# Optimization experiments

Hardware: AMD Instinct MI355X
Metric: run time of the kernel (lower is better)

The kernel has to match this reference:

```python
import jax, jax.numpy as jnp
import numpy as np

H, W = 260, 346          # DAVIS346 sensor resolution
TEMP = 256.0             # time-decay temperature
B, T = 16, 4096          # batch, event sequence length
C = 2 * H + 2 * W        # pred channel dim = 1212


def setup_inputs() -> dict:
    key = jax.random.key(0)
    k1, k2, k3, k4, k5 = jax.random.split(key, 5)
    pred = jax.random.normal(k1, (B, T, C), dtype=jnp.float32)
    # target columns: [timestamp, y_index, x_index, polarity]
    t = jnp.sort(jax.random.uniform(k2, (B, T), minval=0.0, maxval=1.0e6), axis=1)
    y = jax.random.randint(k3, (B, T), 0, H)
    x = jax.random.randint(k4, (B, T), 0, W)
    p = jax.random.randint(k5, (B, T), 0, 2)
    target = jnp.stack([t,
                        y.astype(jnp.float32),
                        x.astype(jnp.float32),
                        p.astype(jnp.float32)], axis=-1)  # [B,T,4]
    return {"pred": pred, "target": target}


def _loss(pred, target):
    t = target[..., 0]                          # [B,T] timestamps
    y = target[..., 1].astype(jnp.int32)        # row indices
    x = target[..., 2].astype(jnp.int32)        # col indices
    p = target[..., 3]                          # polarity in {0,1}
    p_ = p[..., None]

    oh_y = jax.nn.one_hot(y, H, dtype=pred.dtype)   # [B,T,H]
    oh_x = jax.nn.one_hot(x, W, dtype=pred.dtype)   # [B,T,W]
    # scatter targets, concatenated in pred's channel layout [H0|H1|W0|W1]
    base = jnp.concatenate([oh_y * (1.0 - p_), oh_y * p_,
                            oh_x * (1.0 - p_), oh_x * p_], axis=-1)  # [B,T,C]

    # exponential time decay between consecutive events: d_i = exp(-(t_{i+1}-t_i)/TEMP)
    decay = jnp.exp(-(t[:, 1:] - t[:, :-1]) / TEMP)  # [B,T-1]

    # reverse recurrence: s_{T-1} = base_{T-1}; s_i = base_i + d_i * s_{i+1} for i = T-2..1;
    # s_0 = base_0 (torch loop stops before updating index 0)
    base_tm = jnp.swapaxes(base, 0, 1)               # [T,B,C] time-major
    decay_tm = jnp.swapaxes(decay, 0, 1)[..., None]  # [T-1,B,1]

    def step(carry, xd):
        b, d = xd
        s = b + d * carry
        return s, s

    _, ys = jax.lax.scan(step, base_tm[-1], (base_tm[:-1], decay_tm), reverse=True)
    s = jnp.concatenate([ys, base_tm[-1:]], axis=0)  # [T,B,C]
    s = s.at[0].set(base_tm[0])                      # index 0 never accumulated
    s = jnp.swapaxes(s, 0, 1)                        # [B,T,C]

    segs = [(0, H), (H, 2 * H), (2 * H, 2 * H + W), (2 * H + W, C)]
    losses = []
    for a, b in segs:
        logp = jax.nn.log_softmax(pred[..., a:b], axis=-1)
        soft = jax.nn.softmax(s[..., a:b], axis=-1)
        losses.append(-(soft * logp).sum(-1))        # soft-target CE, [B,T]
    lH0, lH1, lW0, lW1 = losses

    loss = ((lH0 + lW0) * (1.0 - p) + (lH1 + lW1) * p).mean()
    return loss


def reference(pred, target):
    return _loss(pred, target)
```

## Files before the change

### kernel.cpp

```cpp
#include <hip/hip_runtime.h>

#define HH 260
#define WW 346
#define CC 1212
#define CP 1280
#define HALF 640
#define NA 606
#define BB 16
#define TT 4096
#define INV_TEMP (1.0f/256.0f)
#define KCH 256
#define LCH 16
#define NG 16
#define GSZ 16
#define GLEN (GSZ * LCH)
#define NJ 10

__global__ __launch_bounds__(256) void p1_local(const float* __restrict__ target,
                                                float* __restrict__ Lbuf) {
    const int blk = blockIdx.x;
    const int b = blk >> 6;
    const int k0 = (blk & 63) << 2;
    const int tid = threadIdx.x;
    const int w = tid >> 6, lane = tid & 63;
    const int k = k0 + w;
    const int a = k * LCH;

    __shared__ float tg[4][LCH][4];
    __shared__ float tnextS[4];
    tg[tid >> 6][(tid >> 2) & 15][tid & 3] =
        target[((size_t)b * TT + k0 * LCH) * 4 + tid];
    if (tid < 4) {
        const int kk = k0 + tid;
        tnextS[tid] = (kk < KCH - 1) ? target[((size_t)b * TT + (kk + 1) * LCH) * 4] : 0.0f;
    }
    __syncthreads();

    float s0[NJ], s1[NJ];
#pragma unroll
    for (int j = 0; j < NJ; ++j) { s0[j] = 0.f; s1[j] = 0.f; }

    for (int li = LCH - 1; li >= 0; --li) {
        const int i = a + li;
        const float ti = tg[w][li][0];
        const float tn = (li == LCH - 1) ? tnextS[w] : tg[w][li + 1][0];
        const float d = (i >= TT - 1) ? 0.0f : __expf(-(tn - ti) * INV_TEMP);
        const int y = (int)tg[w][li][1], x = (int)tg[w][li][2], p = (int)tg[w][li][3];
        const int uy = y, ux = 260 + x;
        if (p == 0) {
#pragma unroll
            for (int j = 0; j < NJ; ++j) {
                const int u = lane + 64 * j;
                const float add = (u == uy ? 1.f : 0.f) + (u == ux ? 1.f : 0.f);
                s0[j] = fmaf(s0[j], d, add);
                s1[j] *= d;
            }
        } else {
#pragma unroll
            for (int j = 0; j < NJ; ++j) {
                const int u = lane + 64 * j;
                const float add = (u == uy ? 1.f : 0.f) + (u == ux ? 1.f : 0.f);
                s1[j] = fmaf(s1[j], d, add);
                s0[j] *= d;
            }
        }
    }
    float* __restrict__ out = Lbuf + (size_t)(b * KCH + k) * CP;
#pragma unroll
    for (int j = 0; j < NJ; ++j) {
        out[lane + 64 * j] = s0[j];
        out[HALF + lane + 64 * j] = s1[j];
    }
}

__global__ __launch_bounds__(256) void p2a(const float* __restrict__ target,
                                           const float* __restrict__ Lbuf,
                                           float* __restrict__ LCin,
                                           float* __restrict__ GroupL) {
    const int blk = blockIdx.x;
    const int ct = blk % 5;
    const int bg = blk / 5;
    const int b = bg >> 4, g = bg & 15;
    const int c = ct * 256 + threadIdx.x;

    float carry = 0.f;
#pragma unroll
    for (int kk = GSZ - 1; kk >= 0; --kk) {
        const int k = g * GSZ + kk;
        const size_t idx = ((size_t)(b * KCH + k)) * CP + c;
        LCin[idx] = carry;
        float P = 0.f;
        if (k < KCH - 1) {
            const float ta = target[((size_t)b * TT + k * LCH) * 4];
            const float te = target[((size_t)b * TT + (k + 1) * LCH) * 4];
            P = __expf(-(te - ta) * INV_TEMP);
        }
        carry = fmaf(P, carry, Lbuf[idx]);
    }
    GroupL[(size_t)bg * CP + c] = carry;
}

__global__ __launch_bounds__(256) void p2b(const float* __restrict__ target,
                                           const float* __restrict__ GroupL,
                                           float* __restrict__ SC) {
    const int blk = blockIdx.x;
    const int ct = blk % 5;
    const int b = blk / 5;
    const int c = ct * 256 + threadIdx.x;

    float Gv[NG], GP[NG];
#pragma unroll
    for (int g = 0; g < NG; ++g)
        Gv[g] = GroupL[((size_t)(b * NG + g)) * CP + c];
#pragma unroll
    for (int g = 0; g < NG; ++g) {
        if (g < NG - 1) {
            const float ta = target[((size_t)b * TT + g * GLEN) * 4];
            const float te = target[((size_t)b * TT + (g + 1) * GLEN) * 4];
            GP[g] = __expf(-(te - ta) * INV_TEMP);
        } else GP[g] = 0.f;
    }
    float carry = 0.f;
#pragma unroll
    for (int g = NG - 1; g >= 0; --g) {
        SC[((size_t)(b * NG + g)) * CP + c] = carry;
        carry = fmaf(GP[g], carry, Gv[g]);
    }
}

__global__ __launch_bounds__(256, 6) void p3_loss(const float* __restrict__ pred,
                                                  const float* __restrict__ target,
                                                  const float* __restrict__ LCin,
                                                  const float* __restrict__ SC,
                                                  double* __restrict__ partials) {
    const int blk = blockIdx.x;
    const int b = blk >> 6;
    const int k0 = (blk & 63) << 2;
    const int tid = threadIdx.x;
    const int w = tid >> 6, lane = tid & 63;
    const int k = k0 + w;
    const int g = k >> 4;
    const int a = k * LCH;

    __shared__ float tg[4][LCH][4];
    __shared__ float tnextS[4];
    tg[tid >> 6][(tid >> 2) & 15][tid & 3] =
        target[((size_t)b * TT + k0 * LCH) * 4 + tid];
    if (tid < 4) {
        const int kk = k0 + tid;
        tnextS[tid] = (kk < KCH - 1) ? target[((size_t)b * TT + (kk + 1) * LCH) * 4] : 0.0f;
    }
    __syncthreads();

    float Qk = 0.f;
    if (g < NG - 1) {
        const float tge = target[((size_t)b * TT + (g + 1) * GLEN) * 4];
        const float tk1 = target[((size_t)b * TT + (k + 1) * LCH) * 4];
        Qk = __expf(-(tge - tk1) * INV_TEMP);
    }

    const float* __restrict__ lc = LCin + (size_t)(b * KCH + k) * CP;
    const float* __restrict__ sc = SC + ((size_t)(b * NG + g)) * CP;
    float s0[NJ], s1[NJ];
#pragma unroll
    for (int j = 0; j < NJ; ++j) {
        const int u = lane + 64 * j;
        s0[j] = fmaf(Qk, sc[u], lc[u]);
        s1[j] = fmaf(Qk, sc[HALF + u], lc[HALF + u]);
    }

    float prA[NJ], prB[NJ];
    {
        const int p = (int)tg[w][LCH - 1][3];
        const float* __restrict__ prow = pred + ((size_t)b * TT + a + LCH - 1) * CC;
#pragma unroll
        for (int j = 0; j < NJ; ++j) {
            const int u = lane + 64 * j;
            const int c = (u < 260) ? p * HH + u : 2 * HH + p * WW + (u - 260);
            prA[j] = (u < NA) ? prow[c] : 0.0f;
        }
    }

    double lacc = 0.0;
    for (int li = LCH - 1; li >= 0; --li) {
        if (li > 0) {
            const int pn = (int)tg[w][li - 1][3];
            const float* __restrict__ prow = pred + ((size_t)b * TT + a + li - 1) * CC;
#pragma unroll
            for (int j = 0; j < NJ; ++j) {
                const int u = lane + 64 * j;
                const int c = (u < 260) ? pn * HH + u : 2 * HH + pn * WW + (u - 260);
                prB[j] = (u < NA) ? prow[c] : 0.0f;
            }
        }

        const int i = a + li;
        const float ti = tg[w][li][0];
        const float tn = (li == LCH - 1) ? tnextS[w] : tg[w][li + 1][0];
        const float d = (i == 0 || i >= TT - 1) ? 0.0f : __expf(-(tn - ti) * INV_TEMP);
        const int y = (int)tg[w][li][1], x = (int)tg[w][li][2], p = (int)tg[w][li][3];
        const int uy = y, ux = 260 + x;

        float zpy = 0.f, zsy = 0.f, dty = 0.f;
        float zpx = 0.f, zsx = 0.f, dtx = 0.f;

        auto stepActive = [&](float (&SA)[NJ], float (&SO)[NJ]) {
#pragma unroll
            for (int j = 0; j < NJ; ++j) {
                const int u = lane + 64 * j;
                const float add = (u == uy ? 1.f : 0.f) + (u == ux ? 1.f : 0.f);
                SA[j] = fmaf(SA[j], d, add);
                SO[j] *= d;
                float es = __expf(SA[j]);
                float ep = __expf(prA[j]);
                if (j == NJ - 1) {
                    const float m = (u < NA) ? 1.f : 0.f;
                    es *= m; ep *= m;
                }
                if (j < 4) {
                    zpy += ep; zsy += es; dty = fmaf(es, prA[j], dty);
                } else if (j == 4) {
                    const bool isY = (u < 260);
                    zpy += isY ? ep : 0.f;
                    zsy += isY ? es : 0.f;
                    dty = fmaf(isY ? es : 0.f, prA[j], dty);
                    zpx += isY ? 0.f : ep;
                    zsx += isY ? 0.f : es;
                    dtx = fmaf(isY ? 0.f : es, prA[j], dtx);
                } else {
                    zpx += ep; zsx += es; dtx = fmaf(es, prA[j], dtx);
                }
            }
        };
        if (p == 0) stepActive(s0, s1); else stepActive(s1, s0);

#pragma unroll
        for (int off = 32; off > 0; off >>= 1) {
            zpy += __shfl_xor(zpy, off);
            zsy += __shfl_xor(zsy, off);
            dty += __shfl_xor(dty, off);
            zpx += __shfl_xor(zpx, off);
            zsx += __shfl_xor(zsx, off);
            dtx += __shfl_xor(dtx, off);
        }
        const float loss = __logf(zpy) + __logf(zpx)
                         - __fdividef(dty, zsy) - __fdividef(dtx, zsx);
        lacc += (double)loss;

#pragma unroll
        for (int j = 0; j < NJ; ++j) prA[j] = prB[j];
    }
    if (lane == 0) partials[b * KCH + k] = lacc;
}

__global__ void p4_final(const double* __restrict__ partials, float* __restrict__ out) {
    const int tid = threadIdx.x;
    double sum = 0.0;
    for (int i = tid; i < BB * KCH; i += 256) sum += partials[i];
#pragma unroll
    for (int off = 32; off > 0; off >>= 1) sum += __shfl_xor(sum, off);
    __shared__ double sred[4];
    if ((tid & 63) == 0) sred[tid >> 6] = sum;
    __syncthreads();
    if (tid == 0)
        out[0] = (float)((sred[0] + sred[1] + sred[2] + sred[3]) / (double)((size_t)BB * TT));
}

extern "C" void kernel_launch(void* const* d_in, const int* in_sizes, int n_in,
                              void* d_out, int out_size, void* d_ws, size_t ws_size,
                              hipStream_t stream) {
    const float* pred   = (const float*)d_in[0];
    const float* target = (const float*)d_in[1];
    float* out = (float*)d_out;

    double* partials = (double*)d_ws;
    float* Lbuf   = (float*)((char*)d_ws + 65536);
    float* LCin   = Lbuf + (size_t)BB * KCH * CP;
    float* GroupL = LCin + (size_t)BB * KCH * CP;
    float* SC     = GroupL + (size_t)BB * NG * CP;

    p1_local<<<BB * KCH / 4, 256, 0, stream>>>(target, Lbuf);
    p2a<<<BB * NG * 5, 256, 0, stream>>>(target, Lbuf, LCin, GroupL);
    p2b<<<BB * 5, 256, 0, stream>>>(target, GroupL, SC);
    p3_loss<<<BB * KCH / 4, 256, 0, stream>>>(pred, target, LCin, SC, partials);
    p4_final<<<1, 256, 0, stream>>>(partials, out);
}
```

Before: 82.13 us.

## Split loss kernel by polarity across a second grid dimension

The loss kernel now launches twice as many blocks, one per polarity half of the state. Each block keeps only one 640-wide state half in registers and processes only the events whose polarity matches its half, decaying the state for the others. The software prefetch of the next pred row is removed and pred is loaded inline. The aim is to halve register state, raise occupancy (launch bounds go from 6 to 8) and give more parallelism, at the cost of exposed pred load latency and possible divergence from data-dependent skipping.

```diff
diff --git a/kernel.cpp b/kernel.cpp
--- a/kernel.cpp
+++ b/kernel.cpp
@@ -128,12 +128,13 @@
     }
 }
 
-__global__ __launch_bounds__(256, 6) void p3_loss(const float* __restrict__ pred,
+__global__ __launch_bounds__(256, 8) void p3_loss(const float* __restrict__ pred,
                                                   const float* __restrict__ target,
                                                   const float* __restrict__ LCin,
                                                   const float* __restrict__ SC,
                                                   double* __restrict__ partials) {
     const int blk = blockIdx.x;
+    const int q = blockIdx.y;
     const int b = blk >> 6;
     const int k0 = (blk & 63) << 2;
     const int tid = threadIdx.x;
@@ -159,80 +160,61 @@
         Qk = __expf(-(tge - tk1) * INV_TEMP);
     }
 
-    const float* __restrict__ lc = LCin + (size_t)(b * KCH + k) * CP;
-    const float* __restrict__ sc = SC + ((size_t)(b * NG + g)) * CP;
-    float s0[NJ], s1[NJ];
+    const float* __restrict__ lc = LCin + (size_t)(b * KCH + k) * CP + q * HALF;
+    const float* __restrict__ sc = SC + ((size_t)(b * NG + g)) * CP + q * HALF;
+    float s[NJ];
 #pragma unroll
     for (int j = 0; j < NJ; ++j) {
         const int u = lane + 64 * j;
-        s0[j] = fmaf(Qk, sc[u], lc[u]);
-        s1[j] = fmaf(Qk, sc[HALF + u], lc[HALF + u]);
-    }
-
-    float prA[NJ], prB[NJ];
-    {
-        const int p = (int)tg[w][LCH - 1][3];
-        const float* __restrict__ prow = pred + ((size_t)b * TT + a + LCH - 1) * CC;
-#pragma unroll
-        for (int j = 0; j < NJ; ++j) {
-            const int u = lane + 64 * j;
-            const int c = (u < 260) ? p * HH + u : 2 * HH + p * WW + (u - 260);
-            prA[j] = (u < NA) ? prow[c] : 0.0f;
-        }
+        s[j] = fmaf(Qk, sc[u], lc[u]);
     }
 
     double lacc = 0.0;
     for (int li = LCH - 1; li >= 0; --li) {
-        if (li > 0) {
-            const int pn = (int)tg[w][li - 1][3];
-            const float* __restrict__ prow = pred + ((size_t)b * TT + a + li - 1) * CC;
-#pragma unroll
-            for (int j = 0; j < NJ; ++j) {
-                const int u = lane + 64 * j;
-                const int c = (u < 260) ? pn * HH + u : 2 * HH + pn * WW + (u - 260);
-                prB[j] = (u < NA) ? prow[c] : 0.0f;
-            }
-        }
-
         const int i = a + li;
         const float ti = tg[w][li][0];
         const float tn = (li == LCH - 1) ? tnextS[w] : tg[w][li + 1][0];
         const float d = (i == 0 || i >= TT - 1) ? 0.0f : __expf(-(tn - ti) * INV_TEMP);
         const int y = (int)tg[w][li][1], x = (int)tg[w][li][2], p = (int)tg[w][li][3];
+
+        if (p != q) {
+#pragma unroll
+            for (int j = 0; j < NJ; ++j) s[j] *= d;
+            continue;
+        }
+
         const int uy = y, ux = 260 + x;
+        const float* __restrict__ prow = pred + ((size_t)b * TT + i) * CC;
 
         float zpy = 0.f, zsy = 0.f, dty = 0.f;
         float zpx = 0.f, zsx = 0.f, dtx = 0.f;
-
-        auto stepActive = [&](float (&SA)[NJ], float (&SO)[NJ]) {
-#pragma unroll
-            for (int j = 0; j < NJ; ++j) {
-                const int u = lane + 64 * j;
-                const float add = (u == uy ? 1.f : 0.f) + (u == ux ? 1.f : 0.f);
-                SA[j] = fmaf(SA[j], d, add);
-                SO[j] *= d;
-                float es = __expf(SA[j]);
-                float ep = __expf(prA[j]);
-                if (j == NJ - 1) {
-                    const float m = (u < NA) ? 1.f : 0.f;
-                    es *= m; ep *= m;
-                }
-                if (j < 4) {
-                    zpy += ep; zsy += es; dty = fmaf(es, prA[j], dty);
-                } else if (j == 4) {
-                    const bool isY = (u < 260);
-                    zpy += isY ? ep : 0.f;
-                    zsy += isY ? es : 0.f;
-                    dty = fmaf(isY ? es : 0.f, prA[j], dty);
-                    zpx += isY ? 0.f : ep;
-                    zsx += isY ? 0.f : es;
-                    dtx = fmaf(isY ? 0.f : es, prA[j], dtx);
-                } else {
-                    zpx += ep; zsx += es; dtx = fmaf(es, prA[j], dtx);
-                }
-            }
-        };
-        if (p == 0) stepActive(s0, s1); else stepActive(s1, s0);
+#pragma unroll
+        for (int j = 0; j < NJ; ++j) {
+            const int u = lane + 64 * j;
+            const float add = (u == uy ? 1.f : 0.f) + (u == ux ? 1.f : 0.f);
+            s[j] = fmaf(s[j], d, add);
+            const int c = (u < 260) ? q * HH + u : 2 * HH + q * WW + (u - 260);
+            const float pr = (u < NA) ? prow[c] : 0.0f;
+            float es = __expf(s[j]);
+            float ep = __expf(pr);
+            if (j == NJ - 1) {
+                const float m = (u < NA) ? 1.f : 0.f;
+                es *= m; ep *= m;
+            }
+            if (j < 4) {
+                zpy += ep; zsy += es; dty = fmaf(es, pr, dty);
+            } else if (j == 4) {
+                const bool isY = (u < 260);
+                zpy += isY ? ep : 0.f;
+                zsy += isY ? es : 0.f;
+                dty = fmaf(isY ? es : 0.f, pr, dty);
+                zpx += isY ? 0.f : ep;
+                zsx += isY ? 0.f : es;
+                dtx = fmaf(isY ? 0.f : es, pr, dtx);
+            } else {
+                zpx += ep; zsx += es; dtx = fmaf(es, pr, dtx);
+            }
+        }
 
 #pragma unroll
         for (int off = 32; off > 0; off >>= 1) {
@@ -246,17 +228,14 @@
         const float loss = __logf(zpy) + __logf(zpx)
                          - __fdividef(dty, zsy) - __fdividef(dtx, zsx);
         lacc += (double)loss;
-
-#pragma unroll
-        for (int j = 0; j < NJ; ++j) prA[j] = prB[j];
-    }
-    if (lane == 0) partials[b * KCH + k] = lacc;
+    }
+    if (lane == 0) partials[q * (BB * KCH) + b * KCH + k] = lacc;
 }
 
 __global__ void p4_final(const double* __restrict__ partials, float* __restrict__ out) {
     const int tid = threadIdx.x;
     double sum = 0.0;
-    for (int i = tid; i < BB * KCH; i += 256) sum += partials[i];
+    for (int i = tid; i < 2 * BB * KCH; i += 256) sum += partials[i];
 #pragma unroll
     for (int off = 32; off > 0; off >>= 1) sum += __shfl_xor(sum, off);
     __shared__ double sred[4];
@@ -282,6 +261,7 @@
     p1_local<<<BB * KCH / 4, 256, 0, stream>>>(target, Lbuf);
     p2a<<<BB * NG * 5, 256, 0, stream>>>(target, Lbuf, LCin, GroupL);
     p2b<<<BB * 5, 256, 0, stream>>>(target, GroupL, SC);
-    p3_loss<<<BB * KCH / 4, 256, 0, stream>>>(pred, target, LCin, SC, partials);
+    dim3 g3(BB * KCH / 4, 2);
+    p3_loss<<<g3, 256, 0, stream>>>(pred, target, LCin, SC, partials);
     p4_final<<<1, 256, 0, stream>>>(partials, out);
 }
```

After: 83.22 us. Within noise of the previous version (+1.3%).
